# Performance work log

Measured on AMD Instinct MI355X. Metric: run time of the kernel, lower is better.

## Reference

```python
import jax, jax.numpy as jnp
import numpy as np

B, N = 256, 65536          # batch, num_tokens (world.num_tokens == N)
VOCAB = 50257
ALPHA = 0.5                # dirichlet concentration
EPS = 1e-7                 # gumbel eps


def setup_inputs() -> dict:
    key = jax.random.key(0)
    kb, kt, ku, kd = jax.random.split(key, 4)
    batch = jax.random.randint(kb, (B, N), 0, VOCAB, dtype=jnp.int32)
    t = jax.random.uniform(kt, (B,), dtype=jnp.float32)
    U = jax.random.uniform(ku, (B, N), dtype=jnp.float32)
    # dirichlet(alpha=0.5) sample over the token axis, one simplex per row
    D = jax.random.dirichlet(kd, ALPHA * jnp.ones((N,), jnp.float32), shape=(B,)).astype(jnp.float32)
    return {"batch": batch, "t": t, "U": U, "D": D}


def cosine_schedule(t):
    return 1.0 - jnp.cos(jnp.pi * t / 2)


def cosine_weight(t, eps=1e-3):
    t_adj = t * (1 - 2 * eps) + eps
    return 0.5 * jnp.pi * jnp.sin(jnp.pi * t_adj / 2)


def binary_topk(weights, ks):
    # weights: [B, N] float; ks: [B, 1] int -> bool mask marking the top-k per row
    Bn, Nn = weights.shape
    idx = jnp.argsort(-weights, axis=-1)                     # descending order indices
    rank = jnp.broadcast_to(jnp.arange(Nn), (Bn, Nn))        # rank of each sorted slot
    mask = jnp.zeros((Bn, Nn), dtype=bool)
    mask = mask.at[jnp.arange(Bn)[:, None], idx].set(ks > rank)
    return mask


def reference(batch, t, U, D):
    r = cosine_schedule(t)                                   # mask rate per sample [B]
    w = cosine_weight(t)                                     # loss weight per sample [B]
    G = -jnp.log(-jnp.log(U + EPS) + EPS)                    # gumbel noise [B, N]
    weights = G + jnp.log(D)                                 # gumbel + log-dirichlet
    ks = (N * r).astype(jnp.int32)[:, None]                  # [B, 1] tokens to mask
    mask = binary_topk(weights, ks)                          # [B, N] bool
    return mask, w
```

## Files before the change

### kernel.cpp

```cpp
#include <hip/hip_runtime.h>
#include <math.h>

#define BB 256
#define NN 65536
#define NTA 256
#define NTB 256
#define NTC 1024
#define SLICES 8
#define SLICE_ELEMS 8192
#define SM 4096
#define RANKPAD 160
#define CAPC 8192
#define BCAP 1024
#define CAPB 2048
#define QMARG 2e-3f

typedef float f32x4 __attribute__((ext_vector_type(4)));
typedef unsigned int u32x4 __attribute__((ext_vector_type(4)));

#define ONE_BITS 0x3F800000u

#define WS_K    0
#define WS_HI   (WS_K + BB)
#define WS_LO   (WS_HI + BB)
#define WS_CAND (WS_LO + BB)
#define WS_A    (WS_CAND + BB)
#define WS_KEYS (WS_A + BB)
#define WS_IDX  (WS_KEYS + BB * CAPC)
#define WS_WORDS ((size_t)WS_IDX + (size_t)BB * CAPC)

__device__ __forceinline__ unsigned int f2sort(float f) {
    unsigned int b = __float_as_uint(f);
    return (b & 0x80000000u) ? ~b : (b | 0x80000000u);
}
__device__ __forceinline__ float sort2f(unsigned int u) {
    unsigned int b = (u & 0x80000000u) ? (u & 0x7fffffffu) : ~u;
    return __uint_as_float(b);
}

__device__ __forceinline__ unsigned int wexact(float u, float d) {
    float t1 = u + 1e-7f;
    float t2 = (float)log((double)t1);
    float t3 = (-t2) + 1e-7f;
    float G  = -(float)log((double)t3);
    float lgD = (float)log((double)d);
    return f2sort(G + lgD);
}

__device__ __forceinline__ unsigned int qkey(float u, float d) {
    float t3 = 1e-7f - __logf(u + 1e-7f);
    float q  = d * __builtin_amdgcn_rcpf(t3);
    return f2sort(q);
}

__device__ __forceinline__ bool finite_f(float f) {
    return (__float_as_uint(f) & 0x7f800000u) != 0x7f800000u;
}

#define PASS1SEL(KKV) \
    { const int b0 = tid * 8; unsigned int cs = 0; \
      _Pragma("unroll") for (int i = 0; i < 8; i++) cs += hist[b0 + i]; \
      chunkSum[tid] = cs; } \
    __syncthreads(); \
    if (tid < 64) { \
        const int c0i = lane * 16; unsigned int s = 0; \
        _Pragma("unroll") for (int i = 0; i < 16; i++) s += chunkSum[c0i + i]; \
        unsigned int suf = s; \
        _Pragma("unroll") for (int off = 1; off < 64; off <<= 1) { \
            unsigned int tv = __shfl_down(suf, off); if (lane + off < 64) suf += tv; } \
        unsigned int above = suf - s; \
        if (suf >= (KKV) && above < (KKV)) { \
            unsigned int cum = above; \
            for (int ci = c0i + 15; ci >= c0i; ci--) { \
                unsigned int cch = chunkSum[ci]; \
                if (cum + cch >= (KKV)) { \
                    for (int b = ci * 8 + 7; ; b--) { \
                        unsigned int c2 = hist[b]; \
                        if (cum + c2 >= (KKV)) { s_sel = (unsigned int)b; s_kneed = (KKV) - cum; s_eq = c2; break; } \
                        cum += c2; } \
                    break; } \
                cum += cch; } } } \
    __syncthreads();

#define PASS2SEL(P, KN) \
    if (tid < 64) { \
        const int c0i = lane * 16; unsigned int s = 0; \
        _Pragma("unroll") for (int i = 0; i < 16; i++) s += hist[c0i + i]; \
        unsigned int suf = s; \
        _Pragma("unroll") for (int off = 1; off < 64; off <<= 1) { \
            unsigned int tv = __shfl_down(suf, off); if (lane + off < 64) suf += tv; } \
        unsigned int above = suf - s; \
        if (suf >= (KN) && above < (KN)) { \
            unsigned int cum = above; \
            for (int b = c0i + 15; ; b--) { \
                unsigned int c2 = hist[b]; \
                if (cum + c2 >= (KN)) { s_sel = ((P) << 10) | (unsigned int)b; s_kneed = (KN) - cum; s_eq = c2; break; } \
                cum += c2; } } } \
    __syncthreads();

#define PASS3SEL(P, KN) \
    if (tid < 64) { \
        const int c0i = lane * 8; unsigned int s = 0; \
        _Pragma("unroll") for (int i = 0; i < 8; i++) s += hist[c0i + i]; \
        unsigned int suf = s; \
        _Pragma("unroll") for (int off = 1; off < 64; off <<= 1) { \
            unsigned int tv = __shfl_down(suf, off); if (lane + off < 64) suf += tv; } \
        unsigned int above = suf - s; \
        if (suf >= (KN) && above < (KN)) { \
            unsigned int cum = above; \
            for (int b = c0i + 7; ; b--) { \
                unsigned int c2 = hist[b]; \
                if (cum + c2 >= (KN)) { s_sel = ((P) << 9) | (unsigned int)b; s_kneed = (KN) - cum; s_eq = c2; break; } \
                cum += c2; } } } \
    __syncthreads();

__device__ __forceinline__ unsigned int rankSelect(const unsigned int* skey,
        unsigned int* h, unsigned int* s_pfx, int* s_need,
        const int tid, const int lane, const int r) {
    if (tid == 0) { *s_pfx = 0u; *s_need = r; }
    __syncthreads();
    for (int shift = 24; shift >= 0; shift -= 8) {
        h[tid] = 0u;
        __syncthreads();
        const unsigned int pfx = *s_pfx;
        const int need = *s_need;
        for (int j = tid; j < SM; j += NTA) {
            const unsigned int sk = skey[j];
            if (shift == 24 || (sk >> (shift + 8)) == (pfx >> (shift + 8)))
                atomicAdd(&h[(sk >> shift) & 255u], 1u);
        }
        __syncthreads();
        if (tid < 64) {
            const int b0 = lane * 4;
            unsigned int s = h[b0] + h[b0 + 1] + h[b0 + 2] + h[b0 + 3];
            unsigned int suf = s;
#pragma unroll
            for (int off = 1; off < 64; off <<= 1) {
                unsigned int tv = __shfl_down(suf, off);
                if (lane + off < 64) suf += tv;
            }
            const unsigned int above = suf - s;
            if (suf >= (unsigned int)need && above < (unsigned int)need) {
                unsigned int cum = above;
                for (int b = b0 + 3; ; b--) {
                    const unsigned int c = h[b];
                    if (cum + c >= (unsigned int)need) {
                        *s_pfx = pfx | ((unsigned int)b << shift);
                        *s_need = need - (int)cum;
                        break;
                    }
                    cum += c;
                }
            }
        }
        __syncthreads();
    }
    return *s_pfx;
}

__global__ __launch_bounds__(NTA)
void md_pivots(const float* __restrict__ Tt, const float* __restrict__ U,
               const float* __restrict__ D, unsigned int* __restrict__ ws,
               float* __restrict__ wout) {
    const int row = blockIdx.x;
    const int tid = threadIdx.x;
    const int lane = tid & 63;

    const float t = Tt[row];
    const float pf = (float)M_PI;
    float bbv = (pf * t) * 0.5f;
    float c0 = (float)cos((double)bbv);
    const int k = (int)(65536.0f * (1.0f - c0));
    if (tid == 0) {
        float tadj = t * 0.998f + 0.001f;
        float arg = (pf * tadj) * 0.5f;
        wout[row] = (float)(0.5 * M_PI) * (float)sin((double)arg);
        ws[WS_K + row] = (unsigned int)k;
        ((int*)ws)[WS_CAND + row] = 0;
        ((int*)ws)[WS_A + row] = 0;
    }
    if (k <= 0 || k >= NN) {
        if (tid == 0) { ws[WS_HI + row] = 0xFFFFFFFFu; ws[WS_LO + row] = 0u; }
        return;
    }

    __shared__ unsigned int skey[SM];
    __shared__ unsigned int h[256];
    __shared__ unsigned int s_pfx;
    __shared__ int s_need;

    const float* Ur = U + (size_t)row * NN;
    const float* Dr = D + (size_t)row * NN;
#pragma unroll
    for (int g = 0; g < 4; ++g) {
        const int e = (g << 10) + (tid << 2);
        float4 u4 = *(const float4*)(Ur + e);
        float4 d4 = *(const float4*)(Dr + e);
        skey[e + 0] = qkey(u4.x, d4.x);
        skey[e + 1] = qkey(u4.y, d4.y);
        skey[e + 2] = qkey(u4.z, d4.z);
        skey[e + 3] = qkey(u4.w, d4.w);
    }
    __syncthreads();

    const int rh = (k >> 4) - RANKPAD;
    const int rl = (k >> 4) + RANKPAD;
    unsigned int hi = 0xFFFFFFFFu;
    unsigned int lo = 0u;
    if (rh >= 1)  hi = rankSelect(skey, h, &s_pfx, &s_need, tid, lane, rh);
    if (rl <= SM) lo = rankSelect(skey, h, &s_pfx, &s_need, tid, lane, rl);
    if (tid == 0) { ws[WS_HI + row] = hi; ws[WS_LO + row] = lo; }
}

__global__ __launch_bounds__(NTB)
void md_stream(const float* __restrict__ U, const float* __restrict__ D,
               float* __restrict__ out, unsigned int* __restrict__ ws) {
    const int bid = blockIdx.x;
    const int row = bid >> 3;
    const int sl = bid & 7;
    const int tid = threadIdx.x;
    const int lane = tid & 63;

    const int k = (int)ws[WS_K + row];
    unsigned int* OrU = (unsigned int*)out + (size_t)row * NN + (size_t)sl * SLICE_ELEMS;
    if (k <= 0 || k >= NN) {
        const unsigned int fv = (k >= NN) ? ONE_BITS : 0u;
        u32x4 f4 = {fv, fv, fv, fv};
        for (int J = 0; J < 8; ++J)
            __builtin_nontemporal_store(f4, (u32x4*)(OrU + (J << 10) + (tid << 2)));
        return;
    }
    const unsigned int hi = ws[WS_HI + row];
    const unsigned int lo = ws[WS_LO + row];
    const float* Ur = U + (size_t)row * NN + (size_t)sl * SLICE_ELEMS;
    const float* Dr = D + (size_t)row * NN + (size_t)sl * SLICE_ELEMS;
    unsigned int* gk = ws + WS_KEYS + (size_t)row * CAPC;
    int* gi = (int*)ws + WS_IDX + (size_t)row * CAPC;
    int* gCand = (int*)ws + WS_CAND + row;
    int* gA = (int*)ws + WS_A + row;

    __shared__ unsigned int lk[BCAP];
    __shared__ int li[BCAP];
    __shared__ int s_cnt, s_base;
    if (tid == 0) s_cnt = 0;
    __syncthreads();

    int dcnt = 0;
    const int ibase = sl * SLICE_ELEMS;
#pragma unroll 2
    for (int J = 0; J < 8; ++J) {
        const int e = (J << 10) + (tid << 2);
        float4 u4 = *(const float4*)(Ur + e);
        float4 d4 = *(const float4*)(Dr + e);
        u32x4 kv;
        kv.x = qkey(u4.x, d4.x); kv.y = qkey(u4.y, d4.y);
        kv.z = qkey(u4.z, d4.z); kv.w = qkey(u4.w, d4.w);
        u32x4 m;
#define SPROC(QV, CI, MF) { const unsigned int qv = (QV); \
        const bool din = qv > hi; dcnt += (int)din; MF = din ? ONE_BITS : 0u; \
        if (!din && qv > lo) { \
            const int p = atomicAdd(&s_cnt, 1); \
            if (p < BCAP) { lk[p] = qv; li[p] = ibase + e + (CI); } \
            else { const int g = atomicAdd(gCand, 1); \
                   if (g < CAPC) { gk[g] = qv; gi[g] = ibase + e + (CI); } } } }
        SPROC(kv.x, 0, m.x)
        SPROC(kv.y, 1, m.y)
        SPROC(kv.z, 2, m.z)
        SPROC(kv.w, 3, m.w)
#undef SPROC
        *(u32x4*)(OrU + e) = m;
    }
#pragma unroll
    for (int off = 32; off >= 1; off >>= 1) dcnt += __shfl_down(dcnt, off);
    if (lane == 0 && dcnt) atomicAdd(gA, dcnt);
    __syncthreads();
    if (tid == 0) {
        int n = s_cnt; if (n > BCAP) n = BCAP;
        s_base = atomicAdd(gCand, n);
    }
    __syncthreads();
    {
        int n = s_cnt; if (n > BCAP) n = BCAP;
        for (int j = tid; j < n; j += NTB) {
            const int g = s_base + j;
            if (g < CAPC) { gk[g] = lk[j]; gi[g] = li[j]; }
        }
    }
}

__global__ __launch_bounds__(NTC)
void md_select(const float* __restrict__ U, const float* __restrict__ D,
               float* __restrict__ out, unsigned int* __restrict__ ws) {
    const int row = blockIdx.x;
    const int tid = threadIdx.x;
    const int lane = tid & 63;

    const int k = (int)ws[WS_K + row];
    if (k <= 0 || k >= NN) return;
    const unsigned int kk = (unsigned int)k;

    const float* Ur = U + (size_t)row * NN;
    const float* Dr = D + (size_t)row * NN;
    unsigned int* OrU = (unsigned int*)out + (size_t)row * NN;

    const unsigned int hi_u = ws[WS_HI + row];
    const unsigned int lo_u = ws[WS_LO + row];
    const int candCnt0 = ((int*)ws)[WS_CAND + row];
    const int A = ((int*)ws)[WS_A + row];
    const unsigned int* gk = ws + WS_KEYS + (size_t)row * CAPC;
    const int* gi = (const int*)ws + WS_IDX + (size_t)row * CAPC;

    __shared__ unsigned int hist[8192];
    __shared__ unsigned int chunkSum[NTC];
    __shared__ unsigned int candKey[CAPC];
    __shared__ int candIdx[CAPC];
    __shared__ unsigned int bandU[CAPB];
    __shared__ int bandIdxA[CAPB];
    __shared__ unsigned int s_sel, s_kneed, s_eq;
    __shared__ int s_bandCnt, s_above, s_tiecnt, s_tieidx;
    int* tielist = candIdx;

    const int kb = k - A;
    bool fb = (candCnt0 > CAPC) || (kb < 1) || (kb > candCnt0);
    const int candCnt = candCnt0 > CAPC ? CAPC : candCnt0;

    unsigned int theta_q = 0, band_lo_u = 0, band_hi_u = 0;
    if (!fb) {
        if (tid == 0) { s_bandCnt = 0; s_above = 0; }
        for (int j = tid; j < candCnt; j += NTC) { candKey[j] = gk[j]; candIdx[j] = gi[j]; }
        for (int i = tid; i < 8192; i += NTC) hist[i] = 0;
        __syncthreads();
        for (int j = tid; j < candCnt; j += NTC) atomicAdd(&hist[candKey[j] >> 19], 1u);
        __syncthreads();
        PASS1SEL((unsigned int)kb)
        const unsigned int c13 = s_sel; const unsigned int ck1 = s_kneed;
        hist[tid] = 0;
        __syncthreads();
        for (int j = tid; j < candCnt; j += NTC) { unsigned int ck = candKey[j];
            if ((ck >> 19) == c13) atomicAdd(&hist[(ck >> 9) & 1023u], 1u); }
        __syncthreads();
        PASS2SEL(c13, ck1)
        const unsigned int c23 = s_sel; const unsigned int ck2 = s_kneed;
        if (tid < 512) hist[tid] = 0;
        __syncthreads();
        for (int j = tid; j < candCnt; j += NTC) { unsigned int ck = candKey[j];
            if ((ck >> 9) == c23) atomicAdd(&hist[ck & 511u], 1u); }
        __syncthreads();
        PASS3SEL(c23, ck2)
        theta_q = s_sel;

        const float theta_f = sort2f(theta_q);
        band_lo_u = f2sort(theta_f * (1.0f - QMARG));
        band_hi_u = f2sort(theta_f * (1.0f + QMARG));
        { const unsigned int fl = (theta_q >= 0x80000100u) ? (theta_q - 256u) : 0x80000000u;
          if (band_lo_u > fl) band_lo_u = fl;
          const unsigned int fh = theta_q + 256u;
          if (band_hi_u < fh) band_hi_u = fh; }
        fb = !(finite_f(theta_f)) || !(band_hi_u < hi_u) || !(band_lo_u > lo_u);
    }

    if (!fb) {
        int ab = 0;
        for (int j = tid; j < candCnt; j += NTC) {
            const unsigned int ck = candKey[j];
            if (ck > band_hi_u) ab++;
            else if (ck >= band_lo_u) {
                const int slot = atomicAdd(&s_bandCnt, 1);
                if (slot < CAPB) bandIdxA[slot] = candIdx[j];
            }
        }
#pragma unroll
        for (int off = 32; off >= 1; off >>= 1) ab += __shfl_down(ab, off);
        if (lane == 0) atomicAdd(&s_above, ab);
        __syncthreads();
        const int bandCnt = s_bandCnt;
        const int kb2 = kb - s_above;
        fb = (bandCnt > CAPB) || (kb2 < 0) || (kb2 > bandCnt);

        if (!fb) {
            for (int j = tid; j < bandCnt; j += NTC) {
                const int idx = bandIdxA[j];
                bandU[j] = wexact(Ur[idx], Dr[idx]);
            }
            __syncthreads();
            for (int j = tid; j < bandCnt; j += NTC) {
                const unsigned int me = bandU[j];
                const int mi = bandIdxA[j];
                int rk = 0;
                for (int i = 0; i < bandCnt; i++) {
                    const unsigned int o = bandU[i];
                    rk += (int)((o > me) || (o == me && bandIdxA[i] < mi));
                }
                if (rk < kb2) OrU[mi] = ONE_BITS;
            }
            for (int j = tid; j < candCnt; j += NTC)
                if (candKey[j] > band_hi_u) OrU[candIdx[j]] = ONE_BITS;
            return;
        }
    }

    __syncthreads();
    for (int i = tid; i < 8192; i += NTC) hist[i] = 0;
    __syncthreads();
#pragma unroll 1
    for (int J = 0; J < 16; ++J) {
        const int e = (J << 12) + (tid << 2);
        float4 u4 = *(const float4*)(Ur + e);
        float4 d4 = *(const float4*)(Dr + e);
        u32x4 kv;
        kv.x = wexact(u4.x, d4.x);
        kv.y = wexact(u4.y, d4.y);
        kv.z = wexact(u4.z, d4.z);
        kv.w = wexact(u4.w, d4.w);
        *(u32x4*)(OrU + e) = kv;
        atomicAdd(&hist[kv.x >> 19], 1u);
        atomicAdd(&hist[kv.y >> 19], 1u);
        atomicAdd(&hist[kv.z >> 19], 1u);
        atomicAdd(&hist[kv.w >> 19], 1u);
    }
    __syncthreads();

    PASS1SEL(kk)
    const unsigned int q13 = s_sel;
    const unsigned int en1 = s_kneed;
    hist[tid] = 0;
    __syncthreads();
#pragma unroll 1
    for (int J = 0; J < 16; ++J) {
        const int e = (J << 12) + (tid << 2);
        u32x4 kv = *(const u32x4*)(OrU + e);
        if ((kv.x >> 19) == q13) atomicAdd(&hist[(kv.x >> 9) & 1023u], 1u);
        if ((kv.y >> 19) == q13) atomicAdd(&hist[(kv.y >> 9) & 1023u], 1u);
        if ((kv.z >> 19) == q13) atomicAdd(&hist[(kv.z >> 9) & 1023u], 1u);
        if ((kv.w >> 19) == q13) atomicAdd(&hist[(kv.w >> 9) & 1023u], 1u);
    }
    __syncthreads();
    PASS2SEL(q13, en1)

    const unsigned int q23 = s_sel;
    const unsigned int en2 = s_kneed;
    if (tid < 512) hist[tid] = 0;
    __syncthreads();
#pragma unroll 1
    for (int J = 0; J < 16; ++J) {
        const int e = (J << 12) + (tid << 2);
        u32x4 kv = *(const u32x4*)(OrU + e);
        if ((kv.x >> 9) == q23) atomicAdd(&hist[kv.x & 511u], 1u);
        if ((kv.y >> 9) == q23) atomicAdd(&hist[kv.y & 511u], 1u);
        if ((kv.z >> 9) == q23) atomicAdd(&hist[kv.z & 511u], 1u);
        if ((kv.w >> 9) == q23) atomicAdd(&hist[kv.w & 511u], 1u);
    }
    __syncthreads();
    PASS3SEL(q23, en2)

    const unsigned int theta = s_sel;
    const unsigned int kneedF = s_kneed, eqF = s_eq;
    const bool needOrder = (kneedF < eqF);
    int istar = NN;
    if (needOrder) {
        if (tid == 0) s_tiecnt = 0;
        __syncthreads();
#pragma unroll 1
        for (int J = 0; J < 16; ++J) {
            const int e = (J << 12) + (tid << 2);
            u32x4 kv = *(const u32x4*)(OrU + e);
#define TIEV(UU, EIDX) if ((UU) == theta) { \
                int pos = atomicAdd(&s_tiecnt, 1); \
                if (pos < 1024) tielist[pos] = (EIDX); }
            TIEV(kv.x, e + 0)
            TIEV(kv.y, e + 1)
            TIEV(kv.z, e + 2)
            TIEV(kv.w, e + 3)
#undef TIEV
        }
        __syncthreads();
        if (tid == 0) {
            int E = s_tiecnt; if (E > 1024) E = 1024;
            for (int aI = 1; aI < E; aI++) {
                int val = tielist[aI]; int bI = aI - 1;
                while (bI >= 0 && tielist[bI] > val) { tielist[bI + 1] = tielist[bI]; bI--; }
                tielist[bI + 1] = val;
            }
            int kk2 = (int)kneedF; if (kk2 > E) kk2 = E; if (kk2 < 1) kk2 = 1;
            s_tieidx = tielist[kk2 - 1];
        }
        __syncthreads();
        istar = s_tieidx;
    }

#pragma unroll 1
    for (int J = 0; J < 16; ++J) {
        const int e = (J << 12) + (tid << 2);
        u32x4 kv = *(const u32x4*)(OrU + e);
        u32x4 m;
#define MVE(u, idx) ((((u) > theta) || ((u) == theta && (!needOrder || (idx) <= istar))) ? ONE_BITS : 0u)
        m.x = MVE(kv.x, e + 0);
        m.y = MVE(kv.y, e + 1);
        m.z = MVE(kv.z, e + 2);
        m.w = MVE(kv.w, e + 3);
#undef MVE
        *(u32x4*)(OrU + e) = m;
    }
}

__global__ __launch_bounds__(NTC, 4)
void md_fused_kernel(const float* __restrict__ Tt,
                     const float* __restrict__ U,
                     const float* __restrict__ D,
                     float* __restrict__ out,
                     float* __restrict__ wout) {
    const int row = blockIdx.x;
    const int tid = threadIdx.x;
    const int lane = tid & 63;

    const float* Ur = U + (size_t)row * NN;
    const float* Dr = D + (size_t)row * NN;
    unsigned int* OrU = (unsigned int*)out + (size_t)row * NN;

    __shared__ unsigned int hist[8192];
    __shared__ unsigned int chunkSum[NTC];
    __shared__ unsigned int skey[SM];
    __shared__ unsigned int candKey[CAPC];
    __shared__ int candIdx[CAPC];
    __shared__ unsigned int s_sel, s_kneed, s_eq;
    __shared__ int s_A, s_candCnt, s_bandCnt, s_above, s_tiecnt, s_tieidx;

    unsigned int* bandU = skey;
    int* bandIdxA = (int*)(skey + CAPB);
    int* tielist = candIdx;

    const float t = Tt[row];
    const float pf = (float)M_PI;
    float bbv = (pf * t) * 0.5f;
    float c0 = (float)cos((double)bbv);
    const int k = (int)(65536.0f * (1.0f - c0));
    if (tid == 0) {
        float tadj = t * 0.998f + 0.001f;
        float arg  = (pf * tadj) * 0.5f;
        wout[row] = (float)(0.5 * M_PI) * (float)sin((double)arg);
    }

    if (k <= 0 || k >= NN) {
        const unsigned int fbv = (k >= NN) ? ONE_BITS : 0u;
        u32x4 f4 = {fbv, fbv, fbv, fbv};
        for (int j = 0; j < 16; j++)
            __builtin_nontemporal_store(f4, (u32x4*)(OrU + j * 4096 + tid * 4));
        return;
    }
    const unsigned int kk = (unsigned int)k;

    for (int i = tid; i < 8192; i += NTC) hist[i] = 0;
    if (tid == 0) { s_A = 0; s_candCnt = 0; s_bandCnt = 0; s_above = 0; }
    __syncthreads();
    {
        float4 u4 = *(const float4*)(Ur + (tid << 2));
        float4 d4 = *(const float4*)(Dr + (tid << 2));
        unsigned int s0 = qkey(u4.x, d4.x), s1 = qkey(u4.y, d4.y);
        unsigned int s2 = qkey(u4.z, d4.z), s3 = qkey(u4.w, d4.w);
        skey[(tid << 2) + 0] = s0; skey[(tid << 2) + 1] = s1;
        skey[(tid << 2) + 2] = s2; skey[(tid << 2) + 3] = s3;
        atomicAdd(&hist[s0 >> 19], 1u); atomicAdd(&hist[s1 >> 19], 1u);
        atomicAdd(&hist[s2 >> 19], 1u); atomicAdd(&hist[s3 >> 19], 1u);
    }
    __syncthreads();

    const int rh = (k >> 4) - RANKPAD;
    unsigned int hi_pivot_u = 0xFFFFFFFFu;
    if (rh >= 1) {
        PASS1SEL((unsigned int)rh)
        const unsigned int bh = s_sel; const unsigned int knh = s_kneed;
        hist[tid] = 0;
        __syncthreads();
        for (int j = tid; j < SM; j += NTC) { unsigned int sk = skey[j];
            if ((sk >> 19) == bh) atomicAdd(&hist[(sk >> 9) & 1023u], 1u); }
        __syncthreads();
        PASS2SEL(bh, knh)
        hi_pivot_u = (s_sel << 9) | 0x1FFu;
        for (int i = tid; i < 8192; i += NTC) hist[i] = 0;
        __syncthreads();
        for (int j = tid; j < SM; j += NTC) atomicAdd(&hist[skey[j] >> 19], 1u);
        __syncthreads();
    }

    const int rl = ((k + 15) >> 4) + RANKPAD;
    unsigned int lo_pivot_u = 0u;
    if (rl <= SM) {
        PASS1SEL((unsigned int)rl)
        const unsigned int bl = s_sel; const unsigned int knl = s_kneed;
        hist[tid] = 0;
        __syncthreads();
        for (int j = tid; j < SM; j += NTC) { unsigned int sk = skey[j];
            if ((sk >> 19) == bl) atomicAdd(&hist[(sk >> 9) & 1023u], 1u); }
        __syncthreads();
        PASS2SEL(bl, knl)
        lo_pivot_u = (s_sel << 9);
    }
    __syncthreads();

    {
        int cntA = 0;
#pragma unroll 2
        for (int J = 0; J < 16; ++J) {
            const int e = (J << 12) + (tid << 2);
            float4 u4 = *(const float4*)(Ur + e);
            float4 d4 = *(const float4*)(Dr + e);
            u32x4 kv;
            kv.x = qkey(u4.x, d4.x); kv.y = qkey(u4.y, d4.y);
            kv.z = qkey(u4.z, d4.z); kv.w = qkey(u4.w, d4.w);
            u32x4 m;
#define MPROC(KC, CI, MF) { \
            const unsigned int qv = (KC); \
            const bool din = qv > hi_pivot_u; \
            cntA += (int)din; MF = din ? ONE_BITS : 0u; \
            if (!din && qv > lo_pivot_u) { \
                int slot = atomicAdd(&s_candCnt, 1); \
                if (slot < CAPC) { candKey[slot] = qv; candIdx[slot] = e + (CI); } } }
            MPROC(kv.x, 0, m.x)
            MPROC(kv.y, 1, m.y)
            MPROC(kv.z, 2, m.z)
            MPROC(kv.w, 3, m.w)
#undef MPROC
            *(u32x4*)(OrU + e) = m;
        }
#pragma unroll
        for (int off = 32; off >= 1; off >>= 1) cntA += __shfl_down(cntA, off);
        if (lane == 0) atomicAdd(&s_A, cntA);
    }
    __syncthreads();

    const int candCnt0 = s_candCnt;
    const int candCnt = candCnt0 > CAPC ? CAPC : candCnt0;
    const int kb = k - s_A;
    bool fb = (candCnt0 > CAPC) || (kb < 1) || (kb > candCnt0);

    unsigned int theta_q = 0, band_lo_u = 0, band_hi_u = 0;
    if (!fb) {
        for (int i = tid; i < 8192; i += NTC) hist[i] = 0;
        __syncthreads();
        for (int j = tid; j < candCnt; j += NTC) atomicAdd(&hist[candKey[j] >> 19], 1u);
        __syncthreads();
        PASS1SEL((unsigned int)kb)
        const unsigned int c13 = s_sel; const unsigned int ck1 = s_kneed;
        hist[tid] = 0;
        __syncthreads();
        for (int j = tid; j < candCnt; j += NTC) { unsigned int ck = candKey[j];
            if ((ck >> 19) == c13) atomicAdd(&hist[(ck >> 9) & 1023u], 1u); }
        __syncthreads();
        PASS2SEL(c13, ck1)
        const unsigned int c23 = s_sel; const unsigned int ck2 = s_kneed;
        if (tid < 512) hist[tid] = 0;
        __syncthreads();
        for (int j = tid; j < candCnt; j += NTC) { unsigned int ck = candKey[j];
            if ((ck >> 9) == c23) atomicAdd(&hist[ck & 511u], 1u); }
        __syncthreads();
        PASS3SEL(c23, ck2)
        theta_q = s_sel;

        const float theta_f = sort2f(theta_q);
        band_lo_u = f2sort(theta_f * (1.0f - QMARG));
        band_hi_u = f2sort(theta_f * (1.0f + QMARG));
        { const unsigned int fl = (theta_q >= 0x80000100u) ? (theta_q - 256u) : 0x80000000u;
          if (band_lo_u > fl) band_lo_u = fl;
          const unsigned int fh = theta_q + 256u;
          if (band_hi_u < fh) band_hi_u = fh; }
        fb = !(finite_f(theta_f)) || !(band_hi_u < hi_pivot_u) || !(band_lo_u > lo_pivot_u);
    }

    if (!fb) {
        int ab = 0;
        for (int j = tid; j < candCnt; j += NTC) {
            const unsigned int ck = candKey[j];
            if (ck > band_hi_u) ab++;
            else if (ck >= band_lo_u) {
                const int slot = atomicAdd(&s_bandCnt, 1);
                if (slot < CAPB) bandIdxA[slot] = candIdx[j];
            }
        }
#pragma unroll
        for (int off = 32; off >= 1; off >>= 1) ab += __shfl_down(ab, off);
        if (lane == 0) atomicAdd(&s_above, ab);
        __syncthreads();
        const int bandCnt = s_bandCnt;
        const int kb2 = kb - s_above;
        fb = (bandCnt > CAPB) || (kb2 < 0) || (kb2 > bandCnt);

        if (!fb) {
            for (int j = tid; j < bandCnt; j += NTC) {
                const int idx = bandIdxA[j];
                bandU[j] = wexact(Ur[idx], Dr[idx]);
            }
            __syncthreads();
            for (int j = tid; j < bandCnt; j += NTC) {
                const unsigned int me = bandU[j];
                const int mi = bandIdxA[j];
                int rk = 0;
                for (int i = 0; i < bandCnt; i++) {
                    const unsigned int o = bandU[i];
                    rk += (int)((o > me) || (o == me && bandIdxA[i] < mi));
                }
                if (rk < kb2) OrU[mi] = ONE_BITS;
            }
            for (int j = tid; j < candCnt; j += NTC)
                if (candKey[j] > band_hi_u) OrU[candIdx[j]] = ONE_BITS;
            return;
        }
    }

    __syncthreads();
    for (int i = tid; i < 8192; i += NTC) hist[i] = 0;
    __syncthreads();
#pragma unroll 1
    for (int J = 0; J < 16; ++J) {
        const int e = (J << 12) + (tid << 2);
        float4 u4 = *(const float4*)(Ur + e);
        float4 d4 = *(const float4*)(Dr + e);
        u32x4 kv;
        kv.x = wexact(u4.x, d4.x);
        kv.y = wexact(u4.y, d4.y);
        kv.z = wexact(u4.z, d4.z);
        kv.w = wexact(u4.w, d4.w);
        *(u32x4*)(OrU + e) = kv;
        atomicAdd(&hist[kv.x >> 19], 1u);
        atomicAdd(&hist[kv.y >> 19], 1u);
        atomicAdd(&hist[kv.z >> 19], 1u);
        atomicAdd(&hist[kv.w >> 19], 1u);
    }
    __syncthreads();

    PASS1SEL(kk)
    const unsigned int q13 = s_sel;
    const unsigned int en1 = s_kneed;
    hist[tid] = 0;
    __syncthreads();
#pragma unroll 1
    for (int J = 0; J < 16; ++J) {
        const int e = (J << 12) + (tid << 2);
        u32x4 kv = *(const u32x4*)(OrU + e);
        if ((kv.x >> 19) == q13) atomicAdd(&hist[(kv.x >> 9) & 1023u], 1u);
        if ((kv.y >> 19) == q13) atomicAdd(&hist[(kv.y >> 9) & 1023u], 1u);
        if ((kv.z >> 19) == q13) atomicAdd(&hist[(kv.z >> 9) & 1023u], 1u);
        if ((kv.w >> 19) == q13) atomicAdd(&hist[(kv.w >> 9) & 1023u], 1u);
    }
    __syncthreads();
    PASS2SEL(q13, en1)

    const unsigned int q23 = s_sel;
    const unsigned int en2 = s_kneed;
    if (tid < 512) hist[tid] = 0;
    __syncthreads();
#pragma unroll 1
    for (int J = 0; J < 16; ++J) {
        const int e = (J << 12) + (tid << 2);
        u32x4 kv = *(const u32x4*)(OrU + e);
        if ((kv.x >> 9) == q23) atomicAdd(&hist[kv.x & 511u], 1u);
        if ((kv.y >> 9) == q23) atomicAdd(&hist[kv.y & 511u], 1u);
        if ((kv.z >> 9) == q23) atomicAdd(&hist[kv.z & 511u], 1u);
        if ((kv.w >> 9) == q23) atomicAdd(&hist[kv.w & 511u], 1u);
    }
    __syncthreads();
    PASS3SEL(q23, en2)

    const unsigned int theta = s_sel;
    const unsigned int kneedF = s_kneed, eqF = s_eq;
    const bool needOrder = (kneedF < eqF);
    int istar = NN;
    if (needOrder) {
        if (tid == 0) s_tiecnt = 0;
        __syncthreads();
#pragma unroll 1
        for (int J = 0; J < 16; ++J) {
            const int e = (J << 12) + (tid << 2);
            u32x4 kv = *(const u32x4*)(OrU + e);
#define TIEV(UU, EIDX) if ((UU) == theta) { \
                int pos = atomicAdd(&s_tiecnt, 1); \
                if (pos < 1024) tielist[pos] = (EIDX); }
            TIEV(kv.x, e + 0)
            TIEV(kv.y, e + 1)
            TIEV(kv.z, e + 2)
            TIEV(kv.w, e + 3)
#undef TIEV
        }
        __syncthreads();
        if (tid == 0) {
            int E = s_tiecnt; if (E > 1024) E = 1024;
            for (int aI = 1; aI < E; aI++) {
                int val = tielist[aI]; int bI = aI - 1;
                while (bI >= 0 && tielist[bI] > val) { tielist[bI + 1] = tielist[bI]; bI--; }
                tielist[bI + 1] = val;
            }
            int kk2 = (int)kneedF; if (kk2 > E) kk2 = E; if (kk2 < 1) kk2 = 1;
            s_tieidx = tielist[kk2 - 1];
        }
        __syncthreads();
        istar = s_tieidx;
    }

#pragma unroll 1
    for (int J = 0; J < 16; ++J) {
        const int e = (J << 12) + (tid << 2);
        u32x4 kv = *(const u32x4*)(OrU + e);
        u32x4 m;
#define MVE(u, idx) ((((u) > theta) || ((u) == theta && (!needOrder || (idx) <= istar))) ? ONE_BITS : 0u)
        m.x = MVE(kv.x, e + 0);
        m.y = MVE(kv.y, e + 1);
        m.z = MVE(kv.z, e + 2);
        m.w = MVE(kv.w, e + 3);
#undef MVE
        *(u32x4*)(OrU + e) = m;
    }
}

extern "C" void kernel_launch(void* const* d_in, const int* in_sizes, int n_in,
                              void* d_out, int out_size, void* d_ws, size_t ws_size,
                              hipStream_t stream) {
    const float* T = (const float*)d_in[1];
    const float* U = (const float*)d_in[2];
    const float* D = (const float*)d_in[3];
    float* out = (float*)d_out;
    float* wout = out + (size_t)BB * NN;

    if (d_ws != nullptr && ws_size >= WS_WORDS * 4ull) {
        unsigned int* ws = (unsigned int*)d_ws;
        md_pivots<<<BB, NTA, 0, stream>>>(T, U, D, ws, wout);
        md_stream<<<BB * SLICES, NTB, 0, stream>>>(U, D, out, ws);
        md_select<<<BB, NTC, 0, stream>>>(U, D, out, ws);
    } else {
        md_fused_kernel<<<BB, NTC, 0, stream>>>(T, U, D, out, wout);
    }
}
```

Before: 248.4 us.

## Fuse selection into stream kernel via last-block-done counter per row

Removes the separate md_select launch. The last of the eight slice blocks for each row, detected with an atomic done counter and thread fences, now runs the candidate radix selection, band ranking and fallback itself. The selection reads candidates straight from global workspace with a 256-thread block instead of staging them in shared memory with 1024 threads. The stream loop also gains register prefetch of upcoming U/D vectors, full unrolling, nontemporal mask stores and an occupancy hint. Risks: the serialized tail work runs on a smaller block, and the band capacity shrinks to BCAP, which makes the slow fallback path more likely.

```diff
diff --git a/kernel.cpp b/kernel.cpp
--- a/kernel.cpp
+++ b/kernel.cpp
@@ -12,7 +12,6 @@
 #define RANKPAD 160
 #define CAPC 8192
 #define BCAP 1024
-#define CAPB 2048
 #define QMARG 2e-3f
 
 typedef float f32x4 __attribute__((ext_vector_type(4)));
@@ -27,7 +26,8 @@
 #define WS_A    (WS_CAND + BB)
 #define WS_KEYS (WS_A + BB)
 #define WS_IDX  (WS_KEYS + BB * CAPC)
-#define WS_WORDS ((size_t)WS_IDX + (size_t)BB * CAPC)
+#define WS_DONE ((size_t)WS_IDX + (size_t)BB * CAPC)
+#define WS_WORDS (WS_DONE + BB)
 
 __device__ __forceinline__ unsigned int f2sort(float f) {
     unsigned int b = __float_as_uint(f);
@@ -56,6 +56,24 @@
 __device__ __forceinline__ bool finite_f(float f) {
     return (__float_as_uint(f) & 0x7f800000u) != 0x7f800000u;
 }
+
+#define RADIX_PICK(PFX, NEED, SHIFT) \
+    if (tid < 64) { \
+        const int b0 = lane * 4; \
+        unsigned int s = h[b0] + h[b0 + 1] + h[b0 + 2] + h[b0 + 3]; \
+        unsigned int suf = s; \
+        _Pragma("unroll") for (int off = 1; off < 64; off <<= 1) { \
+            unsigned int tv = __shfl_down(suf, off); if (lane + off < 64) suf += tv; } \
+        const unsigned int above = suf - s; \
+        if (suf >= (unsigned int)(NEED) && above < (unsigned int)(NEED)) { \
+            unsigned int cum = above; \
+            for (int b = b0 + 3; ; b--) { \
+                const unsigned int c = h[b]; \
+                if (cum + c >= (unsigned int)(NEED)) { \
+                    s_pfx = (PFX) | ((unsigned int)b << (SHIFT)); \
+                    s_need = (NEED) - (int)cum; s_eq = c; break; } \
+                cum += c; } } } \
+    __syncthreads();
 
 #define PASS1SEL(KKV) \
     { const int b0 = tid * 8; unsigned int cs = 0; \
@@ -115,15 +133,15 @@
     __syncthreads();
 
 __device__ __forceinline__ unsigned int rankSelect(const unsigned int* skey,
-        unsigned int* h, unsigned int* s_pfx, int* s_need,
+        unsigned int* h, unsigned int* s_pfxp, int* s_needp,
         const int tid, const int lane, const int r) {
-    if (tid == 0) { *s_pfx = 0u; *s_need = r; }
+    if (tid == 0) { *s_pfxp = 0u; *s_needp = r; }
     __syncthreads();
     for (int shift = 24; shift >= 0; shift -= 8) {
         h[tid] = 0u;
         __syncthreads();
-        const unsigned int pfx = *s_pfx;
-        const int need = *s_need;
+        const unsigned int pfx = *s_pfxp;
+        const int need = *s_needp;
         for (int j = tid; j < SM; j += NTA) {
             const unsigned int sk = skey[j];
             if (shift == 24 || (sk >> (shift + 8)) == (pfx >> (shift + 8)))
@@ -145,8 +163,8 @@
                 for (int b = b0 + 3; ; b--) {
                     const unsigned int c = h[b];
                     if (cum + c >= (unsigned int)need) {
-                        *s_pfx = pfx | ((unsigned int)b << shift);
-                        *s_need = need - (int)cum;
+                        *s_pfxp = pfx | ((unsigned int)b << shift);
+                        *s_needp = need - (int)cum;
                         break;
                     }
                     cum += c;
@@ -155,7 +173,7 @@
         }
         __syncthreads();
     }
-    return *s_pfx;
+    return *s_pfxp;
 }
 
 __global__ __launch_bounds__(NTA)
@@ -178,6 +196,7 @@
         ws[WS_K + row] = (unsigned int)k;
         ((int*)ws)[WS_CAND + row] = 0;
         ((int*)ws)[WS_A + row] = 0;
+        ((int*)ws)[WS_DONE + row] = 0;
     }
     if (k <= 0 || k >= NN) {
         if (tid == 0) { ws[WS_HI + row] = 0xFFFFFFFFu; ws[WS_LO + row] = 0u; }
@@ -212,7 +231,7 @@
     if (tid == 0) { ws[WS_HI + row] = hi; ws[WS_LO + row] = lo; }
 }
 
-__global__ __launch_bounds__(NTB)
+__global__ __launch_bounds__(NTB, 8)
 void md_stream(const float* __restrict__ U, const float* __restrict__ D,
                float* __restrict__ out, unsigned int* __restrict__ ws) {
     const int bid = blockIdx.x;
@@ -222,7 +241,8 @@
     const int lane = tid & 63;
 
     const int k = (int)ws[WS_K + row];
-    unsigned int* OrU = (unsigned int*)out + (size_t)row * NN + (size_t)sl * SLICE_ELEMS;
+    unsigned int* OrUrow = (unsigned int*)out + (size_t)row * NN;
+    unsigned int* OrU = OrUrow + (size_t)sl * SLICE_ELEMS;
     if (k <= 0 || k >= NN) {
         const unsigned int fv = (k >= NN) ? ONE_BITS : 0u;
         u32x4 f4 = {fv, fv, fv, fv};
@@ -238,27 +258,38 @@
     int* gi = (int*)ws + WS_IDX + (size_t)row * CAPC;
     int* gCand = (int*)ws + WS_CAND + row;
     int* gA = (int*)ws + WS_A + row;
+    int* gDone = (int*)ws + WS_DONE + row;
 
     __shared__ unsigned int lk[BCAP];
     __shared__ int li[BCAP];
-    __shared__ int s_cnt, s_base;
+    __shared__ unsigned int h[256];
+    __shared__ unsigned int s_pfx, s_eq;
+    __shared__ int s_need;
+    __shared__ int s_cnt, s_base, s_last, s_above, s_tieidx;
+
     if (tid == 0) s_cnt = 0;
     __syncthreads();
 
+    const f32x4* Uv = (const f32x4*)Ur;
+    const f32x4* Dv = (const f32x4*)Dr;
+    f32x4 u0 = Uv[tid],           d0 = Dv[tid];
+    f32x4 u1 = Uv[tid + NTB],     d1 = Dv[tid + NTB];
+    f32x4 u2 = Uv[tid + 2 * NTB], d2 = Dv[tid + 2 * NTB];
     int dcnt = 0;
     const int ibase = sl * SLICE_ELEMS;
-#pragma unroll 2
+#pragma unroll
     for (int J = 0; J < 8; ++J) {
+        const f32x4 uc = u0, dc = d0;
+        u0 = u1; d0 = d1; u1 = u2; d1 = d2;
+        if (J < 5) { u2 = Uv[tid + (J + 3) * NTB]; d2 = Dv[tid + (J + 3) * NTB]; }
         const int e = (J << 10) + (tid << 2);
-        float4 u4 = *(const float4*)(Ur + e);
-        float4 d4 = *(const float4*)(Dr + e);
         u32x4 kv;
-        kv.x = qkey(u4.x, d4.x); kv.y = qkey(u4.y, d4.y);
-        kv.z = qkey(u4.z, d4.z); kv.w = qkey(u4.w, d4.w);
+        kv.x = qkey(uc.x, dc.x); kv.y = qkey(uc.y, dc.y);
+        kv.z = qkey(uc.z, dc.z); kv.w = qkey(uc.w, dc.w);
         u32x4 m;
 #define SPROC(QV, CI, MF) { const unsigned int qv = (QV); \
-        const bool din = qv > hi; dcnt += (int)din; MF = din ? ONE_BITS : 0u; \
-        if (!din && qv > lo) { \
+        const bool dn = qv > hi; dcnt += (int)dn; MF = dn ? ONE_BITS : 0u; \
+        if (!dn && qv > lo) { \
             const int p = atomicAdd(&s_cnt, 1); \
             if (p < BCAP) { lk[p] = qv; li[p] = ibase + e + (CI); } \
             else { const int g = atomicAdd(gCand, 1); \
@@ -268,87 +299,51 @@
         SPROC(kv.z, 2, m.z)
         SPROC(kv.w, 3, m.w)
 #undef SPROC
-        *(u32x4*)(OrU + e) = m;
+        __builtin_nontemporal_store(m, (u32x4*)(OrU + e));
     }
 #pragma unroll
     for (int off = 32; off >= 1; off >>= 1) dcnt += __shfl_down(dcnt, off);
     if (lane == 0 && dcnt) atomicAdd(gA, dcnt);
     __syncthreads();
-    if (tid == 0) {
-        int n = s_cnt; if (n > BCAP) n = BCAP;
-        s_base = atomicAdd(gCand, n);
-    }
-    __syncthreads();
-    {
-        int n = s_cnt; if (n > BCAP) n = BCAP;
-        for (int j = tid; j < n; j += NTB) {
-            const int g = s_base + j;
-            if (g < CAPC) { gk[g] = lk[j]; gi[g] = li[j]; }
-        }
-    }
-}
-
-__global__ __launch_bounds__(NTC)
-void md_select(const float* __restrict__ U, const float* __restrict__ D,
-               float* __restrict__ out, unsigned int* __restrict__ ws) {
-    const int row = blockIdx.x;
-    const int tid = threadIdx.x;
-    const int lane = tid & 63;
-
-    const int k = (int)ws[WS_K + row];
-    if (k <= 0 || k >= NN) return;
-    const unsigned int kk = (unsigned int)k;
-
-    const float* Ur = U + (size_t)row * NN;
-    const float* Dr = D + (size_t)row * NN;
-    unsigned int* OrU = (unsigned int*)out + (size_t)row * NN;
-
-    const unsigned int hi_u = ws[WS_HI + row];
-    const unsigned int lo_u = ws[WS_LO + row];
-    const int candCnt0 = ((int*)ws)[WS_CAND + row];
-    const int A = ((int*)ws)[WS_A + row];
-    const unsigned int* gk = ws + WS_KEYS + (size_t)row * CAPC;
-    const int* gi = (const int*)ws + WS_IDX + (size_t)row * CAPC;
-
-    __shared__ unsigned int hist[8192];
-    __shared__ unsigned int chunkSum[NTC];
-    __shared__ unsigned int candKey[CAPC];
-    __shared__ int candIdx[CAPC];
-    __shared__ unsigned int bandU[CAPB];
-    __shared__ int bandIdxA[CAPB];
-    __shared__ unsigned int s_sel, s_kneed, s_eq;
-    __shared__ int s_bandCnt, s_above, s_tiecnt, s_tieidx;
-    int* tielist = candIdx;
-
+    if (tid == 0) { int n = s_cnt; if (n > BCAP) n = BCAP; s_base = atomicAdd(gCand, n); }
+    __syncthreads();
+    { int n = s_cnt; if (n > BCAP) n = BCAP;
+      for (int j = tid; j < n; j += NTB) {
+          const int g = s_base + j;
+          if (g < CAPC) { gk[g] = lk[j]; gi[g] = li[j]; } } }
+    __syncthreads();
+    __threadfence();
+    if (tid == 0) s_last = atomicAdd(gDone, 1);
+    __syncthreads();
+    if (s_last != SLICES - 1) return;
+    __threadfence();
+
+    const float* UrR = U + (size_t)row * NN;
+    const float* DrR = D + (size_t)row * NN;
+    const int candCnt0 = *gCand;
+    const int A = *gA;
     const int kb = k - A;
+    const int candCnt = candCnt0 > CAPC ? CAPC : candCnt0;
     bool fb = (candCnt0 > CAPC) || (kb < 1) || (kb > candCnt0);
-    const int candCnt = candCnt0 > CAPC ? CAPC : candCnt0;
-
-    unsigned int theta_q = 0, band_lo_u = 0, band_hi_u = 0;
+
+    unsigned int band_lo_u = 0, band_hi_u = 0;
     if (!fb) {
-        if (tid == 0) { s_bandCnt = 0; s_above = 0; }
-        for (int j = tid; j < candCnt; j += NTC) { candKey[j] = gk[j]; candIdx[j] = gi[j]; }
-        for (int i = tid; i < 8192; i += NTC) hist[i] = 0;
-        __syncthreads();
-        for (int j = tid; j < candCnt; j += NTC) atomicAdd(&hist[candKey[j] >> 19], 1u);
-        __syncthreads();
-        PASS1SEL((unsigned int)kb)
-        const unsigned int c13 = s_sel; const unsigned int ck1 = s_kneed;
-        hist[tid] = 0;
-        __syncthreads();
-        for (int j = tid; j < candCnt; j += NTC) { unsigned int ck = candKey[j];
-            if ((ck >> 19) == c13) atomicAdd(&hist[(ck >> 9) & 1023u], 1u); }
-        __syncthreads();
-        PASS2SEL(c13, ck1)
-        const unsigned int c23 = s_sel; const unsigned int ck2 = s_kneed;
-        if (tid < 512) hist[tid] = 0;
-        __syncthreads();
-        for (int j = tid; j < candCnt; j += NTC) { unsigned int ck = candKey[j];
-            if ((ck >> 9) == c23) atomicAdd(&hist[ck & 511u], 1u); }
-        __syncthreads();
-        PASS3SEL(c23, ck2)
-        theta_q = s_sel;
-
+        if (tid == 0) { s_pfx = 0u; s_need = kb; }
+        __syncthreads();
+        for (int shift = 24; shift >= 0; shift -= 8) {
+            h[tid] = 0u;
+            __syncthreads();
+            const unsigned int pfx = s_pfx;
+            const int need = s_need;
+            for (int j = tid; j < candCnt; j += NTB) {
+                const unsigned int ck = gk[j];
+                if (shift == 24 || (ck >> (shift + 8)) == (pfx >> (shift + 8)))
+                    atomicAdd(&h[(ck >> shift) & 255u], 1u);
+            }
+            __syncthreads();
+            RADIX_PICK(pfx, need, shift)
+        }
+        const unsigned int theta_q = s_pfx;
         const float theta_f = sort2f(theta_q);
         band_lo_u = f2sort(theta_f * (1.0f - QMARG));
         band_hi_u = f2sort(theta_f * (1.0f + QMARG));
@@ -356,142 +351,114 @@
           if (band_lo_u > fl) band_lo_u = fl;
           const unsigned int fh = theta_q + 256u;
           if (band_hi_u < fh) band_hi_u = fh; }
-        fb = !(finite_f(theta_f)) || !(band_hi_u < hi_u) || !(band_lo_u > lo_u);
+        fb = !(finite_f(theta_f)) || !(band_hi_u < hi) || !(band_lo_u > lo);
     }
 
     if (!fb) {
+        if (tid == 0) { s_cnt = 0; s_above = 0; }
+        __syncthreads();
         int ab = 0;
-        for (int j = tid; j < candCnt; j += NTC) {
-            const unsigned int ck = candKey[j];
-            if (ck > band_hi_u) ab++;
+        for (int j = tid; j < candCnt; j += NTB) {
+            const unsigned int ck = gk[j];
+            if (ck > band_hi_u) { ab++; OrUrow[gi[j]] = ONE_BITS; }
             else if (ck >= band_lo_u) {
-                const int slot = atomicAdd(&s_bandCnt, 1);
-                if (slot < CAPB) bandIdxA[slot] = candIdx[j];
+                const int slot = atomicAdd(&s_cnt, 1);
+                if (slot < BCAP) li[slot] = gi[j];
             }
         }
 #pragma unroll
         for (int off = 32; off >= 1; off >>= 1) ab += __shfl_down(ab, off);
         if (lane == 0) atomicAdd(&s_above, ab);
         __syncthreads();
-        const int bandCnt = s_bandCnt;
+        const int bandCnt = s_cnt;
         const int kb2 = kb - s_above;
-        fb = (bandCnt > CAPB) || (kb2 < 0) || (kb2 > bandCnt);
-
+        fb = (bandCnt > BCAP) || (kb2 < 0) || (kb2 > bandCnt);
         if (!fb) {
-            for (int j = tid; j < bandCnt; j += NTC) {
-                const int idx = bandIdxA[j];
-                bandU[j] = wexact(Ur[idx], Dr[idx]);
+            for (int j = tid; j < bandCnt; j += NTB) {
+                const int idx = li[j];
+                lk[j] = wexact(UrR[idx], DrR[idx]);
             }
             __syncthreads();
-            for (int j = tid; j < bandCnt; j += NTC) {
-                const unsigned int me = bandU[j];
-                const int mi = bandIdxA[j];
+            for (int j = tid; j < bandCnt; j += NTB) {
+                const unsigned int me = lk[j];
+                const int mi = li[j];
                 int rk = 0;
                 for (int i = 0; i < bandCnt; i++) {
-                    const unsigned int o = bandU[i];
-                    rk += (int)((o > me) || (o == me && bandIdxA[i] < mi));
+                    const unsigned int o = lk[i];
+                    rk += (int)((o > me) || (o == me && li[i] < mi));
                 }
-                if (rk < kb2) OrU[mi] = ONE_BITS;
-            }
-            for (int j = tid; j < candCnt; j += NTC)
-                if (candKey[j] > band_hi_u) OrU[candIdx[j]] = ONE_BITS;
+                if (rk < kb2) OrUrow[mi] = ONE_BITS;
+            }
             return;
         }
     }
 
     __syncthreads();
-    for (int i = tid; i < 8192; i += NTC) hist[i] = 0;
-    __syncthreads();
-#pragma unroll 1
-    for (int J = 0; J < 16; ++J) {
-        const int e = (J << 12) + (tid << 2);
-        float4 u4 = *(const float4*)(Ur + e);
-        float4 d4 = *(const float4*)(Dr + e);
+    for (int J = 0; J < 64; ++J) {
+        const int e = (J << 10) + (tid << 2);
+        float4 u4 = *(const float4*)(UrR + e);
+        float4 d4 = *(const float4*)(DrR + e);
         u32x4 kv;
-        kv.x = wexact(u4.x, d4.x);
-        kv.y = wexact(u4.y, d4.y);
-        kv.z = wexact(u4.z, d4.z);
-        kv.w = wexact(u4.w, d4.w);
-        *(u32x4*)(OrU + e) = kv;
-        atomicAdd(&hist[kv.x >> 19], 1u);
-        atomicAdd(&hist[kv.y >> 19], 1u);
-        atomicAdd(&hist[kv.z >> 19], 1u);
-        atomicAdd(&hist[kv.w >> 19], 1u);
-    }
-    __syncthreads();
-
-    PASS1SEL(kk)
-    const unsigned int q13 = s_sel;
-    const unsigned int en1 = s_kneed;
-    hist[tid] = 0;
-    __syncthreads();
-#pragma unroll 1
-    for (int J = 0; J < 16; ++J) {
-        const int e = (J << 12) + (tid << 2);
-        u32x4 kv = *(const u32x4*)(OrU + e);
-        if ((kv.x >> 19) == q13) atomicAdd(&hist[(kv.x >> 9) & 1023u], 1u);
-        if ((kv.y >> 19) == q13) atomicAdd(&hist[(kv.y >> 9) & 1023u], 1u);
-        if ((kv.z >> 19) == q13) atomicAdd(&hist[(kv.z >> 9) & 1023u], 1u);
-        if ((kv.w >> 19) == q13) atomicAdd(&hist[(kv.w >> 9) & 1023u], 1u);
-    }
-    __syncthreads();
-    PASS2SEL(q13, en1)
-
-    const unsigned int q23 = s_sel;
-    const unsigned int en2 = s_kneed;
-    if (tid < 512) hist[tid] = 0;
-    __syncthreads();
-#pragma unroll 1
-    for (int J = 0; J < 16; ++J) {
-        const int e = (J << 12) + (tid << 2);
-        u32x4 kv = *(const u32x4*)(OrU + e);
-        if ((kv.x >> 9) == q23) atomicAdd(&hist[kv.x & 511u], 1u);
-        if ((kv.y >> 9) == q23) atomicAdd(&hist[kv.y & 511u], 1u);
-        if ((kv.z >> 9) == q23) atomicAdd(&hist[kv.z & 511u], 1u);
-        if ((kv.w >> 9) == q23) atomicAdd(&hist[kv.w & 511u], 1u);
-    }
-    __syncthreads();
-    PASS3SEL(q23, en2)
-
-    const unsigned int theta = s_sel;
-    const unsigned int kneedF = s_kneed, eqF = s_eq;
-    const bool needOrder = (kneedF < eqF);
+        kv.x = wexact(u4.x, d4.x); kv.y = wexact(u4.y, d4.y);
+        kv.z = wexact(u4.z, d4.z); kv.w = wexact(u4.w, d4.w);
+        *(u32x4*)(OrUrow + e) = kv;
+    }
+    __syncthreads();
+    if (tid == 0) { s_pfx = 0u; s_need = k; s_eq = 0u; }
+    __syncthreads();
+    for (int shift = 24; shift >= 0; shift -= 8) {
+        h[tid] = 0u;
+        __syncthreads();
+        const unsigned int pfx = s_pfx;
+        const int need = s_need;
+        for (int j4 = tid; j4 < (NN >> 2); j4 += NTB) {
+            const u32x4 kv = *(const u32x4*)(OrUrow + (j4 << 2));
+            if (shift == 24) {
+                atomicAdd(&h[kv.x >> 24], 1u); atomicAdd(&h[kv.y >> 24], 1u);
+                atomicAdd(&h[kv.z >> 24], 1u); atomicAdd(&h[kv.w >> 24], 1u);
+            } else {
+                if ((kv.x >> (shift + 8)) == (pfx >> (shift + 8))) atomicAdd(&h[(kv.x >> shift) & 255u], 1u);
+                if ((kv.y >> (shift + 8)) == (pfx >> (shift + 8))) atomicAdd(&h[(kv.y >> shift) & 255u], 1u);
+                if ((kv.z >> (shift + 8)) == (pfx >> (shift + 8))) atomicAdd(&h[(kv.z >> shift) & 255u], 1u);
+                if ((kv.w >> (shift + 8)) == (pfx >> (shift + 8))) atomicAdd(&h[(kv.w >> shift) & 255u], 1u);
+            }
+        }
+        __syncthreads();
+        RADIX_PICK(pfx, need, shift)
+    }
+    const unsigned int theta = s_pfx;
+    const int kneed = s_need;
+    const unsigned int eqc = s_eq;
+    const bool needOrder = (kneed < (int)eqc);
     int istar = NN;
     if (needOrder) {
-        if (tid == 0) s_tiecnt = 0;
-        __syncthreads();
-#pragma unroll 1
-        for (int J = 0; J < 16; ++J) {
-            const int e = (J << 12) + (tid << 2);
-            u32x4 kv = *(const u32x4*)(OrU + e);
-#define TIEV(UU, EIDX) if ((UU) == theta) { \
-                int pos = atomicAdd(&s_tiecnt, 1); \
-                if (pos < 1024) tielist[pos] = (EIDX); }
-            TIEV(kv.x, e + 0)
-            TIEV(kv.y, e + 1)
-            TIEV(kv.z, e + 2)
-            TIEV(kv.w, e + 3)
-#undef TIEV
+        if (tid == 0) s_cnt = 0;
+        __syncthreads();
+        for (int j4 = tid; j4 < (NN >> 2); j4 += NTB) {
+            const u32x4 kv = *(const u32x4*)(OrUrow + (j4 << 2));
+            const int e = j4 << 2;
+            if (kv.x == theta) { int p = atomicAdd(&s_cnt, 1); if (p < BCAP) li[p] = e + 0; }
+            if (kv.y == theta) { int p = atomicAdd(&s_cnt, 1); if (p < BCAP) li[p] = e + 1; }
+            if (kv.z == theta) { int p = atomicAdd(&s_cnt, 1); if (p < BCAP) li[p] = e + 2; }
+            if (kv.w == theta) { int p = atomicAdd(&s_cnt, 1); if (p < BCAP) li[p] = e + 3; }
         }
         __syncthreads();
         if (tid == 0) {
-            int E = s_tiecnt; if (E > 1024) E = 1024;
+            int E = s_cnt; if (E > BCAP) E = BCAP;
             for (int aI = 1; aI < E; aI++) {
-                int val = tielist[aI]; int bI = aI - 1;
-                while (bI >= 0 && tielist[bI] > val) { tielist[bI + 1] = tielist[bI]; bI--; }
-                tielist[bI + 1] = val;
-            }
-            int kk2 = (int)kneedF; if (kk2 > E) kk2 = E; if (kk2 < 1) kk2 = 1;
-            s_tieidx = tielist[kk2 - 1];
+                int val = li[aI]; int bI = aI - 1;
+                while (bI >= 0 && li[bI] > val) { li[bI + 1] = li[bI]; bI--; }
+                li[bI + 1] = val;
+            }
+            int kk2 = kneed; if (kk2 > E) kk2 = E; if (kk2 < 1) kk2 = 1;
+            s_tieidx = li[kk2 - 1];
         }
         __syncthreads();
         istar = s_tieidx;
     }
-
-#pragma unroll 1
-    for (int J = 0; J < 16; ++J) {
-        const int e = (J << 12) + (tid << 2);
-        u32x4 kv = *(const u32x4*)(OrU + e);
+    for (int J = 0; J < 64; ++J) {
+        const int e = (J << 10) + (tid << 2);
+        const u32x4 kv = *(const u32x4*)(OrUrow + e);
         u32x4 m;
 #define MVE(u, idx) ((((u) > theta) || ((u) == theta && (!needOrder || (idx) <= istar))) ? ONE_BITS : 0u)
         m.x = MVE(kv.x, e + 0);
@@ -499,7 +466,7 @@
         m.z = MVE(kv.z, e + 2);
         m.w = MVE(kv.w, e + 3);
 #undef MVE
-        *(u32x4*)(OrU + e) = m;
+        __builtin_nontemporal_store(m, (u32x4*)(OrUrow + e));
     }
 }
 
@@ -526,7 +493,7 @@
     __shared__ int s_A, s_candCnt, s_bandCnt, s_above, s_tiecnt, s_tieidx;
 
     unsigned int* bandU = skey;
-    int* bandIdxA = (int*)(skey + CAPB);
+    int* bandIdxA = (int*)(skey + 2048);
     int* tielist = candIdx;
 
     const float t = Tt[row];
@@ -673,7 +640,7 @@
             if (ck > band_hi_u) ab++;
             else if (ck >= band_lo_u) {
                 const int slot = atomicAdd(&s_bandCnt, 1);
-                if (slot < CAPB) bandIdxA[slot] = candIdx[j];
+                if (slot < 2048) bandIdxA[slot] = candIdx[j];
             }
         }
 #pragma unroll
@@ -682,7 +649,7 @@
         __syncthreads();
         const int bandCnt = s_bandCnt;
         const int kb2 = kb - s_above;
-        fb = (bandCnt > CAPB) || (kb2 < 0) || (kb2 > bandCnt);
+        fb = (bandCnt > 2048) || (kb2 < 0) || (kb2 > bandCnt);
 
         if (!fb) {
             for (int j = tid; j < bandCnt; j += NTC) {
@@ -823,7 +790,6 @@
         unsigned int* ws = (unsigned int*)d_ws;
         md_pivots<<<BB, NTA, 0, stream>>>(T, U, D, ws, wout);
         md_stream<<<BB * SLICES, NTB, 0, stream>>>(U, D, out, ws);
-        md_select<<<BB, NTC, 0, stream>>>(U, D, out, ws);
     } else {
         md_fused_kernel<<<BB, NTC, 0, stream>>>(T, U, D, out, wout);
     }
```

After: 724.8 us. 192% more time.
